# Optimization experiments

Measured on AMD Instinct MI355X. Metric: run time of the kernel, lower is better.

Reference implementation:

```python
import jax, jax.numpy as jnp
import numpy as np

N = 4096
FEAT = 5
H = 128
L = 3
K = 4
HD = H // K  # 32


def setup_inputs() -> dict:
    key = jax.random.key(0)
    ks = jax.random.split(key, 24)
    node_features = jax.random.normal(ks[0], (N, FEAT), dtype=jnp.float32)
    u = jax.random.uniform(ks[1], (N, N), dtype=jnp.float32)
    adj = jnp.where(u < 0.01, u, 0.0)
    adj = adj / (adj.sum(axis=1, keepdims=True) + 1e-8)  # row-normalised
    mask = jax.random.randint(ks[2], (N,), 0, 2).astype(bool)
    s = 0.05
    return {
        'node_features': node_features,
        'adj': adj,
        'mask': mask,
        'Wi': jax.random.normal(ks[3], (FEAT, H), jnp.float32) * s,
        'bi': jnp.zeros((H,), jnp.float32),
        'gat_W': jax.random.normal(ks[4], (L, K, H, HD), jnp.float32) * s,
        'gat_a': jax.random.normal(ks[5], (L, K, 2 * HD), jnp.float32) * s,
        'ln_g': jnp.ones((L, H), jnp.float32),
        'ln_b': jnp.zeros((L, H), jnp.float32),
        'pW1': jax.random.normal(ks[6], (H, H // 2), jnp.float32) * s,
        'pb1': jnp.zeros((H // 2,), jnp.float32),
        'pW2': jax.random.normal(ks[7], (H // 2, 1), jnp.float32) * s,
        'pb2': jnp.zeros((1,), jnp.float32),
        'poolW': jax.random.normal(ks[8], (H, H), jnp.float32) * s,
        'poolb': jnp.zeros((H,), jnp.float32),
        'poolv': jax.random.normal(ks[9], (H,), jnp.float32) * s,
        'vW1': jax.random.normal(ks[10], (H, H // 2), jnp.float32) * s,
        'vb1': jnp.zeros((H // 2,), jnp.float32),
        'vW2': jax.random.normal(ks[11], (H // 2, 1), jnp.float32) * s,
        'vb2': jnp.zeros((1,), jnp.float32),
    }


def _layernorm(x, g, b, eps=1e-5):
    mu = x.mean(-1, keepdims=True)
    var = ((x - mu) ** 2).mean(-1, keepdims=True)
    return (x - mu) / jnp.sqrt(var + eps) * g + b


def reference(node_features, adj, mask, Wi, bi, gat_W, gat_a, ln_g, ln_b,
              pW1, pb1, pW2, pb2, poolW, poolb, poolv, vW1, vb1, vW2, vb2):
    n = node_features.shape[0]
    x = jax.nn.relu(node_features @ Wi + bi)  # (N, H)
    edge_mask = (adj > 0) | jnp.eye(n, dtype=bool)  # (N, N) incl self-loops
    n_layers = gat_W.shape[0]
    for l in range(n_layers):
        Wx = jnp.einsum('nd,kdh->knh', x, gat_W[l])  # (K, N, hd)
        a_src = jnp.einsum('knh,kh->kn', Wx, gat_a[l][:, :HD])  # (K, N)
        a_dst = jnp.einsum('knh,kh->kn', Wx, gat_a[l][:, HD:])  # (K, N)
        e = jax.nn.leaky_relu(a_src[:, :, None] + a_dst[:, None, :], 0.2)  # (K,N,N)
        e = jnp.where(edge_mask[None], e, -jnp.inf)
        alpha = jax.nn.softmax(e, axis=-1)  # softmax over neighbours j
        h = jax.nn.elu(jnp.einsum('kij,kjh->kih', alpha, Wx))  # (K, N, hd)
        out = jnp.transpose(h, (1, 0, 2)).reshape(n, -1)  # concat heads -> (N, H)
        out = out + x  # residual (Identity: in_dim == out_dim)
        x = _layernorm(out, ln_g[l], ln_b[l])
    # policy head
    logits = (jax.nn.relu(x @ pW1 + pb1) @ pW2 + pb2).squeeze(-1)  # (N,)
    logits = jnp.where(mask, logits, -jnp.inf)
    # attention pooling restricted to masked (valid) nodes
    scores = jnp.tanh(x @ poolW + poolb) @ poolv  # (N,)
    scores = jnp.where(mask, scores, -jnp.inf)
    beta = jax.nn.softmax(scores)
    pooled = (beta[:, None] * x).sum(0)  # (H,)
    value = (jax.nn.relu(pooled @ vW1 + vb1) @ vW2 + vb2).squeeze(-1)  # scalar
    return logits, value
```

## Files before the change

### kernel.cpp

```cpp
#include <hip/hip_runtime.h>

#define NN 4096
#define FEAT 5
#define H 128
#define HD 32
#define KH 4
#define NEG_INF (-__builtin_inff())
#define MASK_SENTINEL (-1e30f)

#define WS_FLAG  0
#define WS_DEG   256
#define WS_NBR   (WS_DEG + NN*4)
#define WS_X     (WS_NBR + NN*128*4)
#define WS_WX    (WS_X + NN*H*4)
#define WS_ATS   (WS_WX + NN*H*2)
#define WS_ATD   (WS_ATS + NN*16)
#define WS_PART  (WS_ATD + NN*16)
#define WS_ZPART (WS_PART + 256*H*4)

__device__ __forceinline__ float red64(float v) {
#pragma unroll
    for (int off = 32; off; off >>= 1) v += __shfl_xor(v, off, 64);
    return v;
}
__device__ __forceinline__ float red64max(float v) {
#pragma unroll
    for (int off = 32; off; off >>= 1) v = fmaxf(v, __shfl_xor(v, off, 64));
    return v;
}
__device__ __forceinline__ float red32(float v) {
#pragma unroll
    for (int off = 16; off; off >>= 1) v += __shfl_xor(v, off, 32);
    return v;
}
__device__ __forceinline__ bool read_mask(const void* mp, int f, int n) {
    if (f == 3) return ((const long long*)mp)[n] != 0;
    if (f == 1) return ((const int*)mp)[n] != 0;
    if (f == 2) return ((const float*)mp)[n] != 0.f;
    return ((const unsigned char*)mp)[n] != 0;
}

__global__ __launch_bounds__(256) void k_csr_proj(
    const float* __restrict__ adj, const float* __restrict__ nf,
    const float* __restrict__ Wi, const float* __restrict__ bi,
    const void* mask, int* flag, int* __restrict__ deg,
    int* __restrict__ nbr, float* __restrict__ xbuf) {
    __shared__ int ln[4][128];
    __shared__ unsigned short cand[4][64][12];
    int w = threadIdx.x >> 6, lane = threadIdx.x & 63;
    int row = blockIdx.x * 4 + w;
    ln[w][lane] = 0; ln[w][64 + lane] = 0;
    const float4* arow = (const float4*)(adj + (size_t)row * NN);
    int cnt = 0;
    bool self = false;
#pragma unroll 4
    for (int j = 0; j < 16; j++) {
        float4 v = arow[lane * 16 + j];
        int cb = lane * 64 + j * 4;
        float vals[4] = {v.x, v.y, v.z, v.w};
#pragma unroll
        for (int s = 0; s < 4; s++) {
            if (vals[s] > 0.f) {
                if (cnt < 12) cand[w][lane][cnt] = (unsigned short)(cb + s);
                cnt++;
                if (cb + s == row) self = true;
            }
        }
    }
    int cl = cnt < 12 ? cnt : 12;
    int inc = cl;
#pragma unroll
    for (int off = 1; off < 64; off <<= 1) {
        int o = __shfl_up(inc, off, 64);
        if (lane >= off) inc += o;
    }
    int excl = inc - cl;
    int total = __shfl(inc, 63, 64);
    bool anyself = __any((int)self);
    for (int t2 = 0; t2 < cl; t2++) {
        int pos = excl + t2;
        if (pos < 128) ln[w][pos] = cand[w][lane][t2];
    }
    if (!anyself) {
        if (lane == 0 && total < 128) ln[w][total] = row;
        total++;
    }
    int d = total < 128 ? total : 128;
    if (lane == 0) deg[row] = d;
    nbr[(size_t)row * 128 + lane] = ln[w][lane];
    nbr[(size_t)row * 128 + 64 + lane] = ln[w][64 + lane];
    float a1 = bi[lane], a2 = bi[64 + lane];
#pragma unroll
    for (int f = 0; f < FEAT; f++) {
        float xv = nf[row * FEAT + f];
        a1 += xv * Wi[f * H + lane];
        a2 += xv * Wi[f * H + 64 + lane];
    }
    xbuf[(size_t)row * H + lane] = fmaxf(a1, 0.f);
    xbuf[(size_t)row * H + 64 + lane] = fmaxf(a2, 0.f);
    if (blockIdx.x == 0 && w == 0) {
        const unsigned* ip = (const unsigned*)mask;
        const float* fp = (const float*)mask;
        bool i32ok = true, i64ok = true, f32ok = true;
        for (int i = lane; i < 1024; i += 64) {
            unsigned v = ip[i];
            if (v > 1u) i32ok = false;
            if (i & 1) { if (v != 0u) i64ok = false; }
            else       { if (v > 1u) i64ok = false; }
            float fv = fp[i];
            if (fv != 0.f && fv != 1.f) f32ok = false;
        }
        i32ok = (__ballot((int)i32ok) == ~0ull);
        i64ok = (__ballot((int)i64ok) == ~0ull);
        f32ok = (__ballot((int)f32ok) == ~0ull);
        if (lane == 0) *flag = i64ok ? 3 : (i32ok ? 1 : (f32ok ? 2 : 0));
    }
}

__global__ __launch_bounds__(256) void k_wx(
    const float* __restrict__ xbuf, const float* __restrict__ gw,
    const float* __restrict__ ga, unsigned short* __restrict__ WxBF,
    float* __restrict__ attS, float* __restrict__ attD) {
    __shared__ float xs[8][H];
    int t = threadIdx.x;
    int k = t >> 6, lane = t & 63, dh = lane >> 5, h = lane & 31;
    int n0 = blockIdx.x * 8;
    ((float4*)xs)[t] = ((const float4*)(xbuf + (size_t)n0 * H))[t];
    __syncthreads();
    float acc[8] = {0, 0, 0, 0, 0, 0, 0, 0};
    const float* g = gw + (size_t)k * (H * HD) + h;
    for (int dd = 0; dd < 64; dd += 4) {
        int d = dh * 64 + dd;
        float w0 = g[(size_t)(d + 0) * HD];
        float w1 = g[(size_t)(d + 1) * HD];
        float w2 = g[(size_t)(d + 2) * HD];
        float w3 = g[(size_t)(d + 3) * HD];
#pragma unroll
        for (int nn = 0; nn < 8; nn++) {
            float4 xv = *(const float4*)&xs[nn][d];
            acc[nn] += xv.x * w0 + xv.y * w1 + xv.z * w2 + xv.w * w3;
        }
    }
    float aws = ga[k * 64 + h], awd = ga[k * 64 + 32 + h];
#pragma unroll
    for (int nn = 0; nn < 8; nn++) {
        float full = acc[nn] + __shfl_xor(acc[nn], 32, 64);
        float s = red32(full * aws);
        float dv = red32(full * awd);
        int n = n0 + nn;
        if (dh == 0)
            WxBF[(size_t)n * H + k * 32 + h] =
                (unsigned short)((__float_as_uint(full) + 0x8000u) >> 16);
        if (lane == 0) { attS[n * 4 + k] = s; attD[n * 4 + k] = dv; }
    }
}

__global__ __launch_bounds__(256) void k_agg(
    const int* __restrict__ degG, const int* __restrict__ nbrG,
    const unsigned short* __restrict__ WxBF, const float4* __restrict__ attS4,
    const float4* __restrict__ attD4, const float* __restrict__ lng,
    const float* __restrict__ lnb, float* __restrict__ xbuf) {
    __shared__ float s_al[4][128][4];
    int t = threadIdx.x, w = t >> 6, lane = t & 63;
    int node = blockIdx.x * 4 + w;
    int d = degG[node];
    const int* np = nbrG + (size_t)node * 128;
    int sn0 = np[lane], sn1 = np[64 + lane];
    float4 aS = attS4[node];
    float4 d0 = attD4[sn0], d1 = attD4[sn1];
    bool v0 = lane < d, v1 = 64 + lane < d;
#define LRELU(x) ((x) > 0.f ? (x) : 0.2f * (x))
    float e0x = v0 ? LRELU(aS.x + d0.x) : NEG_INF;
    float e0y = v0 ? LRELU(aS.y + d0.y) : NEG_INF;
    float e0z = v0 ? LRELU(aS.z + d0.z) : NEG_INF;
    float e0w = v0 ? LRELU(aS.w + d0.w) : NEG_INF;
    float e1x = v1 ? LRELU(aS.x + d1.x) : NEG_INF;
    float e1y = v1 ? LRELU(aS.y + d1.y) : NEG_INF;
    float e1z = v1 ? LRELU(aS.z + d1.z) : NEG_INF;
    float e1w = v1 ? LRELU(aS.w + d1.w) : NEG_INF;
#undef LRELU
    float mx = red64max(fmaxf(e0x, e1x));
    float my = red64max(fmaxf(e0y, e1y));
    float mz = red64max(fmaxf(e0z, e1z));
    float mw = red64max(fmaxf(e0w, e1w));
    float p0x = v0 ? __expf(e0x - mx) : 0.f, p1x = v1 ? __expf(e1x - mx) : 0.f;
    float p0y = v0 ? __expf(e0y - my) : 0.f, p1y = v1 ? __expf(e1y - my) : 0.f;
    float p0z = v0 ? __expf(e0z - mz) : 0.f, p1z = v1 ? __expf(e1z - mz) : 0.f;
    float p0w = v0 ? __expf(e0w - mw) : 0.f, p1w = v1 ? __expf(e1w - mw) : 0.f;
    float ix = 1.f / red64(p0x + p1x);
    float iy = 1.f / red64(p0y + p1y);
    float iz = 1.f / red64(p0z + p1z);
    float iw = 1.f / red64(p0w + p1w);
    *(float4*)&s_al[w][lane][0]      = make_float4(p0x * ix, p0y * iy, p0z * iz, p0w * iw);
    *(float4*)&s_al[w][64 + lane][0] = make_float4(p1x * ix, p1y * iy, p1z * iz, p1w * iw);
    int ksel = lane >> 4;
    float acc0 = 0.f, acc1 = 0.f;
    int dpad = (d + 7) & ~7;
    for (int c0 = 0; c0 < dpad; c0 += 8) {
#pragma unroll
        for (int j = 0; j < 8; j++) {
            int c = c0 + j;
            int sc = np[c];
            float4 a4 = *(const float4*)&s_al[w][c][0];
            float al = ksel == 0 ? a4.x : ksel == 1 ? a4.y : ksel == 2 ? a4.z : a4.w;
            unsigned v = *((const unsigned*)(WxBF + (size_t)sc * H) + lane);
            acc0 += al * __uint_as_float(v << 16);
            acc1 += al * __uint_as_float(v & 0xFFFF0000u);
        }
    }
    int dim0 = 2 * lane;
    float2 xr = *(const float2*)(xbuf + (size_t)node * H + dim0);
    float h0 = acc0 > 0.f ? acc0 : __expf(acc0) - 1.f;
    float h1 = acc1 > 0.f ? acc1 : __expf(acc1) - 1.f;
    float o0 = h0 + xr.x, o1 = h1 + xr.y;
    float mu = red64(o0 + o1) * (1.f / H);
    float dv0 = o0 - mu, dv1 = o1 - mu;
    float var = red64(dv0 * dv0 + dv1 * dv1) * (1.f / H);
    float rstd = rsqrtf(var + 1e-5f);
    float2 ov;
    ov.x = dv0 * rstd * lng[dim0] + lnb[dim0];
    ov.y = dv1 * rstd * lng[dim0 + 1] + lnb[dim0 + 1];
    *(float2*)(xbuf + (size_t)node * H + dim0) = ov;
}

__global__ __launch_bounds__(256) void k_heads(
    const float* __restrict__ xbuf, const float* __restrict__ pW1,
    const float* __restrict__ pb1, const float* __restrict__ pW2,
    const float* __restrict__ pb2, const float* __restrict__ poolW,
    const float* __restrict__ poolb, const float* __restrict__ poolv,
    const void* mask, const int* __restrict__ flag, float* __restrict__ out,
    float* __restrict__ part, float* __restrict__ zpart) {
    __shared__ float lds_x[16][H];
    __shared__ float lds_part[4][H];
    __shared__ float lds_z[4];
    int t = threadIdx.x, w = t >> 6, lane = t & 63;
    int n0b = blockIdx.x * 16;
    for (int idx = t; idx < 16 * H; idx += 256)
        lds_x[idx >> 7][idx & 127] = xbuf[(size_t)(n0b + (idx >> 7)) * H + (idx & 127)];
    __syncthreads();
    int nb = n0b + w * 4;
    float accp[4] = {0, 0, 0, 0}, acs1[4] = {0, 0, 0, 0}, acs2[4] = {0, 0, 0, 0};
#pragma unroll 2
    for (int d = 0; d < H; d++) {
        float w1 = pW1[d * 64 + lane];
        float q1 = poolW[d * H + lane];
        float q2 = poolW[d * H + 64 + lane];
#pragma unroll
        for (int nn = 0; nn < 4; nn++) {
            float xv = lds_x[w * 4 + nn][d];
            accp[nn] += xv * w1;
            acs1[nn] += xv * q1;
            acs2[nn] += xv * q2;
        }
    }
    int flg = *flag;
    float T = fminf(red64(fabsf(poolv[lane]) + fabsf(poolv[64 + lane])), 30.f);
    float pb1v = pb1[lane], pw2v = pW2[lane], pb2v = pb2[0];
    float pob1 = poolb[lane], pob2 = poolb[64 + lane];
    float pov1 = poolv[lane], pov2 = poolv[64 + lane];
    float pp1 = 0.f, pp2 = 0.f, zacc = 0.f;
#pragma unroll
    for (int nn = 0; nn < 4; nn++) {
        int node = nb + nn;
        float hp = red64(fmaxf(accp[nn] + pb1v, 0.f) * pw2v);
        float sc = red64(tanhf(acs1[nn] + pob1) * pov1 + tanhf(acs2[nn] + pob2) * pov2);
        bool mk = read_mask(mask, flg, node);
        if (lane == 0) out[node] = mk ? (hp + pb2v) : MASK_SENTINEL;
        float wn = mk ? __expf(sc - T) : 0.f;
        pp1 += wn * lds_x[w * 4 + nn][lane];
        pp2 += wn * lds_x[w * 4 + nn][64 + lane];
        zacc += wn;
    }
    lds_part[w][lane] = pp1;
    lds_part[w][64 + lane] = pp2;
    if (lane == 0) lds_z[w] = zacc;
    __syncthreads();
    if (w == 0) {
        float s1 = lds_part[0][lane] + lds_part[1][lane] + lds_part[2][lane] + lds_part[3][lane];
        float s2 = lds_part[0][64 + lane] + lds_part[1][64 + lane] +
                   lds_part[2][64 + lane] + lds_part[3][64 + lane];
        part[blockIdx.x * H + lane] = s1;
        part[blockIdx.x * H + 64 + lane] = s2;
        if (lane == 0) zpart[blockIdx.x] = lds_z[0] + lds_z[1] + lds_z[2] + lds_z[3];
    }
}

__global__ __launch_bounds__(1024) void k_value(
    const float* __restrict__ part, const float* __restrict__ zpart,
    const float* __restrict__ vW1, const float* __restrict__ vb1,
    const float* __restrict__ vW2, const float* __restrict__ vb2,
    float* __restrict__ out) {
    __shared__ float segsum[8][H];
    __shared__ float zfin[256];
    __shared__ float pooled[H];
    int t = threadIdx.x;
    int dim = t & 127, seg = t >> 7;
    float s = 0.f;
#pragma unroll 8
    for (int b = seg * 32; b < seg * 32 + 32; b++) s += part[b * H + dim];
    segsum[seg][dim] = s;
    if (t < 256) zfin[t] = zpart[t];
    __syncthreads();
    if (t < 512) {
        int sg = t >> 7;
        segsum[sg][dim] += segsum[sg + 4][dim];
    }
    if (t >= 512 && t < 640) zfin[t - 512] += zfin[t - 512 + 128];
    __syncthreads();
    if (t < 256) {
        int sg = t >> 7;
        segsum[sg][dim] += segsum[sg + 2][dim];
    }
    if (t >= 512 && t < 576) zfin[t - 512] += zfin[t - 512 + 64];
    __syncthreads();
    if (t < 128) segsum[0][dim] += segsum[1][dim];
    if (t >= 512 && t < 544) zfin[t - 512] += zfin[t - 512 + 32];
    __syncthreads();
    if (t < 32) {
        float z = zfin[t];
#pragma unroll
        for (int off = 16; off; off >>= 1) z += __shfl_xor(z, off, 32);
        if (t == 0) zfin[0] = z;
    }
    __syncthreads();
    float Z = zfin[0];
    if (t < H) pooled[t] = segsum[0][t] / Z;
    __syncthreads();
    if (t < 64) {
        float acc = vb1[t];
#pragma unroll 4
        for (int d = 0; d < H; d++) acc += pooled[d] * vW1[d * 64 + t];
        float v = red64(fmaxf(acc, 0.f) * vW2[t]);
        if (t == 0) out[NN] = v + vb2[0];
    }
}

extern "C" void kernel_launch(void* const* d_in, const int* in_sizes, int n_in,
                              void* d_out, int out_size, void* d_ws, size_t ws_size,
                              hipStream_t stream) {
    const float* nf    = (const float*)d_in[0];
    const float* adj   = (const float*)d_in[1];
    const void*  mask  = d_in[2];
    const float* Wi    = (const float*)d_in[3];
    const float* bi    = (const float*)d_in[4];
    const float* gat_W = (const float*)d_in[5];
    const float* gat_a = (const float*)d_in[6];
    const float* ln_g  = (const float*)d_in[7];
    const float* ln_b  = (const float*)d_in[8];
    const float* pW1   = (const float*)d_in[9];
    const float* pb1   = (const float*)d_in[10];
    const float* pW2   = (const float*)d_in[11];
    const float* pb2   = (const float*)d_in[12];
    const float* poolW = (const float*)d_in[13];
    const float* poolb = (const float*)d_in[14];
    const float* poolv = (const float*)d_in[15];
    const float* vW1   = (const float*)d_in[16];
    const float* vb1   = (const float*)d_in[17];
    const float* vW2   = (const float*)d_in[18];
    const float* vb2   = (const float*)d_in[19];

    char* ws = (char*)d_ws;
    int*            flag = (int*)(ws + WS_FLAG);
    int*            deg  = (int*)(ws + WS_DEG);
    int*            nbr  = (int*)(ws + WS_NBR);
    float*          xbuf = (float*)(ws + WS_X);
    unsigned short* WxBF = (unsigned short*)(ws + WS_WX);
    float* ats   = (float*)(ws + WS_ATS);
    float* atd   = (float*)(ws + WS_ATD);
    float* partb = (float*)(ws + WS_PART);
    float* zpart = (float*)(ws + WS_ZPART);
    float* out   = (float*)d_out;

    const size_t GWL = KH * H * HD;
    const size_t GAL = KH * 2 * HD;

    k_csr_proj<<<1024, 256, 0, stream>>>(adj, nf, Wi, bi, mask, flag, deg, nbr, xbuf);
    for (int l = 0; l < 3; l++) {
        k_wx<<<512, 256, 0, stream>>>(xbuf, gat_W + l * GWL, gat_a + l * GAL,
                                      WxBF, ats, atd);
        k_agg<<<1024, 256, 0, stream>>>(deg, nbr, WxBF, (const float4*)ats,
                                        (const float4*)atd, ln_g + l * H,
                                        ln_b + l * H, xbuf);
    }
    k_heads<<<256, 256, 0, stream>>>(xbuf, pW1, pb1, pW2, pb2, poolW, poolb, poolv,
                                     mask, flag, out, partb, zpart);
    k_value<<<1, 1024, 0, stream>>>(partb, zpart, vW1, vb1, vW2, vb2, out);
}
```

Baseline: 177.1 us.

## Aggregate each node with a full block, staging neighbor rows in LDS

Result: slower. 194.1 us (+9.6%).

```diff
diff --git a/kernel.cpp b/kernel.cpp
--- a/kernel.cpp
+++ b/kernel.cpp
@@ -160,67 +160,105 @@
     const unsigned short* __restrict__ WxBF, const float4* __restrict__ attS4,
     const float4* __restrict__ attD4, const float* __restrict__ lng,
     const float* __restrict__ lnb, float* __restrict__ xbuf) {
-    __shared__ float s_al[4][128][4];
+    __shared__ int      s_nbr[128];
+    __shared__ unsigned s_wx[128][65];
+    __shared__ float    s_al[128][4];
+    __shared__ float    s_m[2][4], s_s[2][4];
+    __shared__ float    s_o[H];
+    __shared__ float    s_r[2], s_r2[2];
     int t = threadIdx.x, w = t >> 6, lane = t & 63;
-    int node = blockIdx.x * 4 + w;
+    int node = blockIdx.x;
     int d = degG[node];
-    const int* np = nbrG + (size_t)node * 128;
-    int sn0 = np[lane], sn1 = np[64 + lane];
+    if (t < 128) s_nbr[t] = nbrG[(size_t)node * 128 + t];
+    __syncthreads();
+    float4 dd4 = make_float4(0.f, 0.f, 0.f, 0.f);
+    if (t < 128) dd4 = attD4[s_nbr[t]];
+    {
+        int base = w * 32;
+#pragma unroll 8
+        for (int i = 0; i < 32; i++) {
+            int c = base + i;
+            int sc = s_nbr[c];
+            unsigned v = *((const unsigned*)(WxBF + (size_t)sc * H) + lane);
+            s_wx[c][lane] = v;
+        }
+    }
     float4 aS = attS4[node];
-    float4 d0 = attD4[sn0], d1 = attD4[sn1];
-    bool v0 = lane < d, v1 = 64 + lane < d;
+    float e0 = NEG_INF, e1 = NEG_INF, e2 = NEG_INF, e3 = NEG_INF;
+    if (t < 128 && t < d) {
 #define LRELU(x) ((x) > 0.f ? (x) : 0.2f * (x))
-    float e0x = v0 ? LRELU(aS.x + d0.x) : NEG_INF;
-    float e0y = v0 ? LRELU(aS.y + d0.y) : NEG_INF;
-    float e0z = v0 ? LRELU(aS.z + d0.z) : NEG_INF;
-    float e0w = v0 ? LRELU(aS.w + d0.w) : NEG_INF;
-    float e1x = v1 ? LRELU(aS.x + d1.x) : NEG_INF;
-    float e1y = v1 ? LRELU(aS.y + d1.y) : NEG_INF;
-    float e1z = v1 ? LRELU(aS.z + d1.z) : NEG_INF;
-    float e1w = v1 ? LRELU(aS.w + d1.w) : NEG_INF;
+        e0 = LRELU(aS.x + dd4.x);
+        e1 = LRELU(aS.y + dd4.y);
+        e2 = LRELU(aS.z + dd4.z);
+        e3 = LRELU(aS.w + dd4.w);
 #undef LRELU
-    float mx = red64max(fmaxf(e0x, e1x));
-    float my = red64max(fmaxf(e0y, e1y));
-    float mz = red64max(fmaxf(e0z, e1z));
-    float mw = red64max(fmaxf(e0w, e1w));
-    float p0x = v0 ? __expf(e0x - mx) : 0.f, p1x = v1 ? __expf(e1x - mx) : 0.f;
-    float p0y = v0 ? __expf(e0y - my) : 0.f, p1y = v1 ? __expf(e1y - my) : 0.f;
-    float p0z = v0 ? __expf(e0z - mz) : 0.f, p1z = v1 ? __expf(e1z - mz) : 0.f;
-    float p0w = v0 ? __expf(e0w - mw) : 0.f, p1w = v1 ? __expf(e1w - mw) : 0.f;
-    float ix = 1.f / red64(p0x + p1x);
-    float iy = 1.f / red64(p0y + p1y);
-    float iz = 1.f / red64(p0z + p1z);
-    float iw = 1.f / red64(p0w + p1w);
-    *(float4*)&s_al[w][lane][0]      = make_float4(p0x * ix, p0y * iy, p0z * iz, p0w * iw);
-    *(float4*)&s_al[w][64 + lane][0] = make_float4(p1x * ix, p1y * iy, p1z * iz, p1w * iw);
-    int ksel = lane >> 4;
+    }
+    if (t < 128) {
+        float m0 = red64max(e0), m1 = red64max(e1);
+        float m2 = red64max(e2), m3 = red64max(e3);
+        if (lane == 0) {
+            s_m[w][0] = m0; s_m[w][1] = m1; s_m[w][2] = m2; s_m[w][3] = m3;
+        }
+    }
+    __syncthreads();
+    if (t < 128) {
+        float m0 = fmaxf(s_m[0][0], s_m[1][0]);
+        float m1 = fmaxf(s_m[0][1], s_m[1][1]);
+        float m2 = fmaxf(s_m[0][2], s_m[1][2]);
+        float m3 = fmaxf(s_m[0][3], s_m[1][3]);
+        bool v = t < d;
+        float p0 = v ? __expf(e0 - m0) : 0.f;
+        float p1 = v ? __expf(e1 - m1) : 0.f;
+        float p2 = v ? __expf(e2 - m2) : 0.f;
+        float p3 = v ? __expf(e3 - m3) : 0.f;
+        *(float4*)&s_al[t][0] = make_float4(p0, p1, p2, p3);
+        float q0 = red64(p0), q1 = red64(p1), q2 = red64(p2), q3 = red64(p3);
+        if (lane == 0) {
+            s_s[w][0] = q0; s_s[w][1] = q1; s_s[w][2] = q2; s_s[w][3] = q3;
+        }
+    }
+    __syncthreads();
+    int p = lane & 15, q = lane >> 4;
+    float inv = 1.f / (s_s[0][w] + s_s[1][w]);
     float acc0 = 0.f, acc1 = 0.f;
-    int dpad = (d + 7) & ~7;
-    for (int c0 = 0; c0 < dpad; c0 += 8) {
-#pragma unroll
-        for (int j = 0; j < 8; j++) {
-            int c = c0 + j;
-            int sc = np[c];
-            float4 a4 = *(const float4*)&s_al[w][c][0];
-            float al = ksel == 0 ? a4.x : ksel == 1 ? a4.y : ksel == 2 ? a4.z : a4.w;
-            unsigned v = *((const unsigned*)(WxBF + (size_t)sc * H) + lane);
-            acc0 += al * __uint_as_float(v << 16);
-            acc1 += al * __uint_as_float(v & 0xFFFF0000u);
-        }
-    }
-    int dim0 = 2 * lane;
-    float2 xr = *(const float2*)(xbuf + (size_t)node * H + dim0);
-    float h0 = acc0 > 0.f ? acc0 : __expf(acc0) - 1.f;
-    float h1 = acc1 > 0.f ? acc1 : __expf(acc1) - 1.f;
-    float o0 = h0 + xr.x, o1 = h1 + xr.y;
-    float mu = red64(o0 + o1) * (1.f / H);
-    float dv0 = o0 - mu, dv1 = o1 - mu;
-    float var = red64(dv0 * dv0 + dv1 * dv1) * (1.f / H);
-    float rstd = rsqrtf(var + 1e-5f);
-    float2 ov;
-    ov.x = dv0 * rstd * lng[dim0] + lnb[dim0];
-    ov.y = dv1 * rstd * lng[dim0 + 1] + lnb[dim0 + 1];
-    *(float2*)(xbuf + (size_t)node * H + dim0) = ov;
+#pragma unroll 8
+    for (int j = 0; j < 32; j++) {
+        int c = 4 * j + q;
+        float al = s_al[c][w];
+        unsigned v = s_wx[c][w * 16 + p];
+        acc0 += al * __uint_as_float(v << 16);
+        acc1 += al * __uint_as_float(v & 0xFFFF0000u);
+    }
+    acc0 += __shfl_xor(acc0, 16, 64); acc0 += __shfl_xor(acc0, 32, 64);
+    acc1 += __shfl_xor(acc1, 16, 64); acc1 += __shfl_xor(acc1, 32, 64);
+    if (lane < 16) {
+        int dim0 = w * 32 + 2 * p;
+        float a0 = acc0 * inv, a1 = acc1 * inv;
+        float h0 = a0 > 0.f ? a0 : __expf(a0) - 1.f;
+        float h1 = a1 > 0.f ? a1 : __expf(a1) - 1.f;
+        float2 xr = *(const float2*)(xbuf + (size_t)node * H + dim0);
+        s_o[dim0] = h0 + xr.x;
+        s_o[dim0 + 1] = h1 + xr.y;
+    }
+    __syncthreads();
+    float o = (t < 128) ? s_o[t] : 0.f;
+    if (t < 128) {
+        float r = red64(o);
+        if (lane == 0) s_r[w] = r;
+    }
+    __syncthreads();
+    float mu = (s_r[0] + s_r[1]) * (1.f / H);
+    float dv = o - mu;
+    if (t < 128) {
+        float vs = red64(dv * dv);
+        if (lane == 0) s_r2[w] = vs;
+    }
+    __syncthreads();
+    if (t < 128) {
+        float var = (s_r2[0] + s_r2[1]) * (1.f / H);
+        float rstd = rsqrtf(var + 1e-5f);
+        xbuf[(size_t)node * H + t] = dv * rstd * lng[t] + lnb[t];
+    }
 }
 
 __global__ __launch_bounds__(256) void k_heads(
@@ -378,7 +416,7 @@
     for (int l = 0; l < 3; l++) {
         k_wx<<<512, 256, 0, stream>>>(xbuf, gat_W + l * GWL, gat_a + l * GAL,
                                       WxBF, ats, atd);
-        k_agg<<<1024, 256, 0, stream>>>(deg, nbr, WxBF, (const float4*)ats,
+        k_agg<<<4096, 256, 0, stream>>>(deg, nbr, WxBF, (const float4*)ats,
                                         (const float4*)atd, ln_g + l * H,
                                         ln_b + l * H, xbuf);
     }
```
